# Performance work log

Hardware: AMD Instinct MI355X
Metric: run time of the kernel (lower is better)

## Reference

```python
import jax, jax.numpy as jnp
import numpy as np

N = 100000      # nodes
E = 1600000     # edges (unique, no self-loops)
DIN = 128
DOUT = 128


def _make_edges():
    """Unique undirected edges, no self-loops, ring guarantees min degree 2.
    Ensures dense-adjacency semantics == edge-list segment-sum semantics."""
    rng = np.random.default_rng(0)
    ring = np.stack([np.arange(N, dtype=np.int64), (np.arange(N, dtype=np.int64) + 1) % N], axis=1)
    ring = np.sort(ring, axis=1)  # canonical (min,max)
    ring_keys = ring[:, 0] * N + ring[:, 1]
    cand = rng.integers(0, N, size=(3 * E, 2), dtype=np.int64)
    cand = cand[cand[:, 0] != cand[:, 1]]
    cand = np.sort(cand, axis=1)
    keys = cand[:, 0] * N + cand[:, 1]
    _, idx = np.unique(keys, return_index=True)
    cand = cand[np.sort(idx)]
    cand = cand[~np.isin(cand[:, 0] * N + cand[:, 1], ring_keys)][: E - N]
    edges = np.concatenate([ring, cand], axis=0)  # [E, 2]
    return edges.T  # [2, E]


def setup_inputs() -> dict:
    key = jax.random.key(0)
    kx, kw = jax.random.split(key)
    X = jax.random.normal(kx, (N, DIN), dtype=jnp.float32)
    # kaiming_normal_ default (fan_in mode): std = sqrt(2 / fan_in)
    W = jax.random.normal(kw, (DIN, DOUT), dtype=jnp.float32) * np.float32(np.sqrt(2.0 / DIN))
    edge_list = jnp.asarray(_make_edges(), dtype=jnp.int64)
    return {"X": X, "W": W, "edge_list": edge_list}


def reference(X, W, edge_list):
    src, dst = edge_list[0], edge_list[1]
    n = X.shape[0]
    ones = jnp.ones(src.shape[0], dtype=X.dtype)
    # D: each edge increments both endpoint degrees (matches the torch loop)
    deg = jnp.zeros((n,), X.dtype).at[src].add(ones).at[dst].add(ones)
    # A_hat @ X = symmetric neighbor aggregation + self (identity)
    agg = jnp.zeros_like(X).at[dst].add(X[src]).at[src].add(X[dst]) + X
    # D^-1 is inverse of diagonal -> elementwise reciprocal
    z = (agg / deg[:, None]) @ W
    return jax.nn.relu(z)
```

## Files before the change

### kernel.cpp

```cpp
#include <hip/hip_runtime.h>
#include <hip/hip_fp16.h>


#define DFEAT 128
#define BSH 7
#define BNODES (1 << BSH)
#define NBMAX 800
#define EPB 8192
#define SORT_CAP 6144
#define EPT (SORT_CAP / 1024)

typedef __attribute__((ext_vector_type(8))) short short8;
typedef __attribute__((ext_vector_type(4))) float f32x4;

__device__ __forceinline__ unsigned short f2bf(float x) {
  unsigned u = __float_as_uint(x);
  return (unsigned short)((u + 0x7FFFu + ((u >> 16) & 1u)) >> 16);
}
__device__ __forceinline__ __half2 u2h(unsigned x) {
  union { unsigned u; __half2 h; } c; c.u = x; return c.h;
}

__global__ void init_kernel(const int* el32, int* gcur, int* flag, int NB) {
  int i = blockIdx.x * blockDim.x + threadIdx.x;
  if (i < NB) gcur[i] = 0;
  if (i == 0) flag[0] = (el32[1] == 0 && el32[3] == 0) ? 1 : 0;
}

__device__ __forceinline__ int edge_at(const void* el, long long i, int mode64) {
  if (mode64) return (int)((const long long*)el)[i];
  return ((const int*)el)[i];
}

__global__ __launch_bounds__(1024) void scatter_kernel(const void* el,
                                                       const int* __restrict__ flag,
                                                       int* __restrict__ gcur,
                                                       unsigned int* __restrict__ bucket,
                                                       int E, int NB) {
  __shared__ int lh[NBMAX];
  __shared__ int lb[NBMAX];
  int t = threadIdx.x;
  for (int i = t; i < NB; i += 1024) lh[i] = 0;
  __syncthreads();
  int m = flag[0];
  long long e0 = (long long)blockIdx.x * EPB + t;
  int s[8], d[8];
#pragma unroll
  for (int r = 0; r < 8; r++) {
    long long e = e0 + r * 1024;
    if (e < E) {
      s[r] = edge_at(el, e, m);
      d[r] = edge_at(el, (long long)E + e, m);
    } else {
      s[r] = -1;
    }
  }
#pragma unroll
  for (int r = 0; r < 8; r++) {
    if (s[r] >= 0) {
      atomicAdd(&lh[s[r] >> BSH], 1);
      atomicAdd(&lh[d[r] >> BSH], 1);
    }
  }
  __syncthreads();
  for (int i = t; i < NB; i += 1024) {
    int c = lh[i];
    lb[i] = c ? atomicAdd(&gcur[i], c) : 0;
  }
  __syncthreads();
  for (int i = t; i < NB; i += 1024) lh[i] = 0;
  __syncthreads();
#pragma unroll
  for (int r = 0; r < 8; r++) {
    if (s[r] >= 0) {
      int bs = s[r] >> BSH, bd = d[r] >> BSH;
      int ps = lb[bs] + atomicAdd(&lh[bs], 1);
      if (ps < SORT_CAP)
        bucket[(long long)bs * SORT_CAP + ps] =
            ((unsigned)(s[r] & (BNODES - 1)) << 20) | (unsigned)d[r];
      int pd = lb[bd] + atomicAdd(&lh[bd], 1);
      if (pd < SORT_CAP)
        bucket[(long long)bd * SORT_CAP + pd] =
            ((unsigned)(d[r] & (BNODES - 1)) << 20) | (unsigned)s[r];
    }
  }
}

__global__ __launch_bounds__(256) void wfrag_kernel(const float* __restrict__ W,
                                                    unsigned int* __restrict__ Wfrag) {
  int e = blockIdx.x * 256 + threadIdx.x;
  if (e >= 2048) return;
  int lane = e & 63;
  int nt = (e >> 6) & 7;
  int kc = e >> 9;
  int k0 = kc * 32 + (lane >> 4) * 8;
  int col = nt * 16 + (lane & 15);
  unsigned int o[4];
#pragma unroll
  for (int jj = 0; jj < 4; jj++) {
    unsigned short lo = f2bf(W[(k0 + 2 * jj) * DFEAT + col]);
    unsigned short hi = f2bf(W[(k0 + 2 * jj + 1) * DFEAT + col]);
    o[jj] = (unsigned)lo | ((unsigned)hi << 16);
  }
  uint4* dst = (uint4*)Wfrag;
  uint4 v; v.x = o[0]; v.y = o[1]; v.z = o[2]; v.w = o[3];
  dst[e] = v;
}

__global__ __launch_bounds__(256) void gemm_kernel(const float* __restrict__ X,
                                                   const short8* __restrict__ Wfrag,
                                                   __half* __restrict__ Yh, int n) {
  int wave = threadIdx.x >> 6;
  int lane = threadIdx.x & 63;
  int row0 = (blockIdx.x * 4 + wave) * 16;
  if (row0 >= n) return;

  int rowA = row0 + (lane & 15);
  if (rowA >= n) rowA = n - 1;
  const float4* Xrow = (const float4*)(X + (long long)rowA * DFEAT);
  int koff = (lane >> 4) * 2;

  f32x4 acc[8];
#pragma unroll
  for (int ntp = 0; ntp < 8; ntp++) acc[ntp] = (f32x4){0.f, 0.f, 0.f, 0.f};

#pragma unroll
  for (int kc = 0; kc < 4; kc++) {
    float4 xa = Xrow[kc * 8 + koff];
    float4 xb = Xrow[kc * 8 + koff + 1];
    short8 a8;
    a8[0] = (short)f2bf(xa.x); a8[1] = (short)f2bf(xa.y);
    a8[2] = (short)f2bf(xa.z); a8[3] = (short)f2bf(xa.w);
    a8[4] = (short)f2bf(xb.x); a8[5] = (short)f2bf(xb.y);
    a8[6] = (short)f2bf(xb.z); a8[7] = (short)f2bf(xb.w);
#pragma unroll
    for (int nt = 0; nt < 8; nt++) {
      short8 b8 = Wfrag[(kc * 8 + nt) * 64 + lane];
      acc[nt] = __builtin_amdgcn_mfma_f32_16x16x32_bf16(a8, b8, acc[nt], 0, 0, 0);
    }
  }

  int rbase = row0 + (lane >> 4) * 4;
  int cbase = lane & 15;
#pragma unroll
  for (int nt = 0; nt < 8; nt++) {
#pragma unroll
    for (int r = 0; r < 4; r++) {
      int row = rbase + r;
      if (row < n)
        Yh[(long long)row * DFEAT + nt * 16 + cbase] = __float2half(acc[nt][r]);
    }
  }
}

__global__ __launch_bounds__(1024) void gather_fused(
    const unsigned int* __restrict__ bucket,
    const int* __restrict__ gcur,
    const unsigned int* __restrict__ Yh,
    float2* __restrict__ out2, int n) {
  __shared__ int srt[SORT_CAP];
  __shared__ int h[BNODES], pref[BNODES], cur[BNODES], scn[BNODES];
  int b = blockIdx.x, t = threadIdx.x;
  int cnt = gcur[b]; if (cnt > SORT_CAP) cnt = SORT_CAP;
  long long base = (long long)b * SORT_CAP;

  if (t < BNODES) h[t] = 0;
  __syncthreads();

  unsigned ent[EPT];
#pragma unroll
  for (int r = 0; r < EPT; r++) {
    int i = t + r * 1024;
    if (i < cnt) {
      unsigned e = bucket[base + i];
      ent[r] = e;
      atomicAdd(&h[e >> 20], 1);
    } else {
      ent[r] = 0xFFFFFFFFu;
    }
  }
  __syncthreads();

  int v = (t < BNODES) ? h[t] : 0;
  if (t < BNODES) scn[t] = v;
  __syncthreads();
  for (int dd = 1; dd < BNODES; dd <<= 1) {
    int a = (t < BNODES && t >= dd) ? scn[t - dd] : 0;
    __syncthreads();
    if (t < BNODES) scn[t] += a;
    __syncthreads();
  }
  if (t < BNODES) { pref[t] = scn[t] - v; cur[t] = scn[t] - v; }
  __syncthreads();

#pragma unroll
  for (int r = 0; r < EPT; r++) {
    unsigned e = ent[r];
    if (e != 0xFFFFFFFFu) {
      int p = atomicAdd(&cur[e >> 20], 1);
      srt[p] = (int)(e & 0xFFFFFu);
    }
  }
  __syncthreads();

  int wave = t >> 6, lane = t & 63;
  int node0 = b << BSH;
#pragma unroll 1
  for (int q = 0; q < 8; q++) {
    int r = wave * 8 + q;
    int node = node0 + r;
    if (node >= n) break;
    int st = pref[r], len = h[r];
    __half2 acc0 = u2h(Yh[(long long)node * 64 + lane]);
    __half2 acc1 = u2h(0);

    for (int bb = 0; bb < len; bb += 64) {
      int c2 = len - bb; if (c2 > 64) c2 = 64;
      int idx = (lane < c2) ? srt[st + bb + lane] : 0;
      int tt = 0;
      for (; tt + 8 <= c2; tt += 8) {
        unsigned vv[8];
#pragma unroll
        for (int u = 0; u < 8; u++) {
          int j = __shfl(idx, tt + u);
          vv[u] = Yh[(long long)j * 64 + lane];
        }
        acc0 = __hadd2(acc0, u2h(vv[0])); acc1 = __hadd2(acc1, u2h(vv[1]));
        acc0 = __hadd2(acc0, u2h(vv[2])); acc1 = __hadd2(acc1, u2h(vv[3]));
        acc0 = __hadd2(acc0, u2h(vv[4])); acc1 = __hadd2(acc1, u2h(vv[5]));
        acc0 = __hadd2(acc0, u2h(vv[6])); acc1 = __hadd2(acc1, u2h(vv[7]));
      }
      for (; tt < c2; tt++) {
        int j = __shfl(idx, tt);
        acc0 = __hadd2(acc0, u2h(Yh[(long long)j * 64 + lane]));
      }
    }

    float2 f0 = __half22float2(acc0);
    float2 f1 = __half22float2(acc1);
    float inv = 1.0f / (float)len;
    float2 o;
    o.x = (f0.x + f1.x) * inv;
    o.y = (f0.y + f1.y) * inv;
    o.x = o.x > 0.f ? o.x : 0.f;
    o.y = o.y > 0.f ? o.y : 0.f;
    out2[(long long)node * 64 + lane] = o;
  }
}

extern "C" void kernel_launch(void* const* d_in, const int* in_sizes, int n_in,
                              void* d_out, int out_size, void* d_ws, size_t ws_size,
                              hipStream_t stream) {
  const float* X = (const float*)d_in[0];
  const float* W = (const float*)d_in[1];
  const void* el = d_in[2];
  float* out = (float*)d_out;

  int n = in_sizes[0] / DFEAT;
  int E = in_sizes[2] / 2;
  int NB = (n + BNODES - 1) >> BSH;

  char* p = (char*)d_ws;
  auto alloc = [&](size_t bytes) -> char* {
    char* q = p;
    p += (bytes + 511) & ~(size_t)511;
    return q;
  };
  int* gcur = (int*)alloc((size_t)NBMAX * 4);
  int* flag = (int*)alloc(64);
  unsigned int* bucket = (unsigned int*)alloc((size_t)NBMAX * SORT_CAP * 4);
  unsigned int* Wfrag = (unsigned int*)alloc((size_t)2048 * 16);
  __half* Yh = (__half*)alloc((size_t)n * DFEAT * 2);

  int eblocks = (E + EPB - 1) / EPB;

  init_kernel<<<(NBMAX + 255) / 256, 256, 0, stream>>>((const int*)el, gcur, flag, NB);
  scatter_kernel<<<eblocks, 1024, 0, stream>>>(el, flag, gcur, bucket, E, NB);
  wfrag_kernel<<<8, 256, 0, stream>>>(W, Wfrag);
  gemm_kernel<<<(n + 63) / 64, 256, 0, stream>>>(X, (const short8*)Wfrag, Yh, n);
  gather_fused<<<NB, 1024, 0, stream>>>(bucket, gcur, (const unsigned int*)Yh,
                                        (float2*)out, n);
}
```

Baseline: 275.6 us.

## Window-partition neighbor lists so gather waves sweep source windows for cache locality

A new sort kernel orders each node bucket's neighbors by a (node, source-window) key and writes per-node, per-window offsets and degrees to global memory. The gather kernel then gives each wave 17 nodes and walks the 16 source windows in order, so concurrent gathers touch one window of Yh at a time and stay in L2. The W-fragment kernel is merged into setup, and scatter uses 4 edges per thread instead of 8. The cost is an extra kernel and pass over the buckets. The gather also loses its 8-way unrolled independent loads, which may lower memory-level parallelism.

Result: slower. 551.4 us (+100.0%).

```diff
diff --git a/kernel.cpp b/kernel.cpp
--- a/kernel.cpp
+++ b/kernel.cpp
@@ -6,9 +6,14 @@
 #define BSH 7
 #define BNODES (1 << BSH)
 #define NBMAX 800
-#define EPB 8192
+#define EPT_SC 4
+#define EPB (1024 * EPT_SC)
 #define SORT_CAP 6144
-#define EPT (SORT_CAP / 1024)
+#define WSH 13
+#define NWSLOT 16
+#define KBINS (BNODES * NWSLOT)
+#define NPW 17
+#define GBLK 1536
 
 typedef __attribute__((ext_vector_type(8))) short short8;
 typedef __attribute__((ext_vector_type(4))) float f32x4;
@@ -21,10 +26,30 @@
   union { unsigned u; __half2 h; } c; c.u = x; return c.h;
 }
 
-__global__ void init_kernel(const int* el32, int* gcur, int* flag, int NB) {
-  int i = blockIdx.x * blockDim.x + threadIdx.x;
-  if (i < NB) gcur[i] = 0;
-  if (i == 0) flag[0] = (el32[1] == 0 && el32[3] == 0) ? 1 : 0;
+__global__ __launch_bounds__(256) void setup_kernel(const int* el32, int* gcur,
+                                                    int* flag,
+                                                    const float* __restrict__ W,
+                                                    unsigned int* __restrict__ Wfrag) {
+  int e = blockIdx.x * 256 + threadIdx.x;
+  if (e < NBMAX) gcur[e] = 0;
+  if (e == 0) flag[0] = (el32[1] == 0 && el32[3] == 0) ? 1 : 0;
+  if (e < 2048) {
+    int lane = e & 63;
+    int nt = (e >> 6) & 7;
+    int kc = e >> 9;
+    int k0 = kc * 32 + (lane >> 4) * 8;
+    int col = nt * 16 + (lane & 15);
+    unsigned int o[4];
+#pragma unroll
+    for (int jj = 0; jj < 4; jj++) {
+      unsigned short lo = f2bf(W[(k0 + 2 * jj) * DFEAT + col]);
+      unsigned short hi = f2bf(W[(k0 + 2 * jj + 1) * DFEAT + col]);
+      o[jj] = (unsigned)lo | ((unsigned)hi << 16);
+    }
+    uint4* dst = (uint4*)Wfrag;
+    uint4 v; v.x = o[0]; v.y = o[1]; v.z = o[2]; v.w = o[3];
+    dst[e] = v;
+  }
 }
 
 __device__ __forceinline__ int edge_at(const void* el, long long i, int mode64) {
@@ -44,9 +69,9 @@
   __syncthreads();
   int m = flag[0];
   long long e0 = (long long)blockIdx.x * EPB + t;
-  int s[8], d[8];
-#pragma unroll
-  for (int r = 0; r < 8; r++) {
+  int s[EPT_SC], d[EPT_SC];
+#pragma unroll
+  for (int r = 0; r < EPT_SC; r++) {
     long long e = e0 + r * 1024;
     if (e < E) {
       s[r] = edge_at(el, e, m);
@@ -56,7 +81,7 @@
     }
   }
 #pragma unroll
-  for (int r = 0; r < 8; r++) {
+  for (int r = 0; r < EPT_SC; r++) {
     if (s[r] >= 0) {
       atomicAdd(&lh[s[r] >> BSH], 1);
       atomicAdd(&lh[d[r] >> BSH], 1);
@@ -71,7 +96,7 @@
   for (int i = t; i < NB; i += 1024) lh[i] = 0;
   __syncthreads();
 #pragma unroll
-  for (int r = 0; r < 8; r++) {
+  for (int r = 0; r < EPT_SC; r++) {
     if (s[r] >= 0) {
       int bs = s[r] >> BSH, bd = d[r] >> BSH;
       int ps = lb[bs] + atomicAdd(&lh[bs], 1);
@@ -86,25 +111,64 @@
   }
 }
 
-__global__ __launch_bounds__(256) void wfrag_kernel(const float* __restrict__ W,
-                                                    unsigned int* __restrict__ Wfrag) {
-  int e = blockIdx.x * 256 + threadIdx.x;
-  if (e >= 2048) return;
-  int lane = e & 63;
-  int nt = (e >> 6) & 7;
-  int kc = e >> 9;
-  int k0 = kc * 32 + (lane >> 4) * 8;
-  int col = nt * 16 + (lane & 15);
-  unsigned int o[4];
-#pragma unroll
-  for (int jj = 0; jj < 4; jj++) {
-    unsigned short lo = f2bf(W[(k0 + 2 * jj) * DFEAT + col]);
-    unsigned short hi = f2bf(W[(k0 + 2 * jj + 1) * DFEAT + col]);
-    o[jj] = (unsigned)lo | ((unsigned)hi << 16);
-  }
-  uint4* dst = (uint4*)Wfrag;
-  uint4 v; v.x = o[0]; v.y = o[1]; v.z = o[2]; v.w = o[3];
-  dst[e] = v;
+__global__ __launch_bounds__(1024) void sortwin_kernel(unsigned int* __restrict__ bucket,
+                                                       const int* __restrict__ gcur,
+                                                       int2* __restrict__ pw,
+                                                       int* __restrict__ degg,
+                                                       int n) {
+  __shared__ int srt[SORT_CAP];
+  __shared__ int h2[KBINS], pr2[KBINS], cur2[KBINS];
+  __shared__ int wsc[1024];
+  int b = blockIdx.x, t = threadIdx.x;
+  int cnt = gcur[b]; if (cnt > SORT_CAP) cnt = SORT_CAP;
+  long long base = (long long)b * SORT_CAP;
+
+  h2[t] = 0; h2[t + 1024] = 0;
+  __syncthreads();
+  for (int i = t; i < cnt; i += 1024) {
+    unsigned e = bucket[base + i];
+    int key = (int)((e >> 20) << 4) | (int)((e & 0xFFFFFu) >> WSH);
+    atomicAdd(&h2[key], 1);
+  }
+  __syncthreads();
+  int a0 = h2[2 * t], a1 = h2[2 * t + 1];
+  int s = a0 + a1;
+  wsc[t] = s;
+  __syncthreads();
+  for (int dd = 1; dd < 1024; dd <<= 1) {
+    int aa = (t >= dd) ? wsc[t - dd] : 0;
+    __syncthreads();
+    wsc[t] += aa;
+    __syncthreads();
+  }
+  int excl = wsc[t] - s;
+  pr2[2 * t] = excl;          cur2[2 * t] = excl;
+  pr2[2 * t + 1] = excl + a0; cur2[2 * t + 1] = excl + a0;
+  __syncthreads();
+  for (int i = t; i < cnt; i += 1024) {
+    unsigned e = bucket[base + i];
+    int key = (int)((e >> 20) << 4) | (int)((e & 0xFFFFFu) >> WSH);
+    int p = atomicAdd(&cur2[key], 1);
+    srt[p] = (int)(e & 0xFFFFFu);
+  }
+  __syncthreads();
+  for (int i = t; i < cnt; i += 1024) bucket[base + i] = (unsigned)srt[i];
+  int node0 = b << BSH;
+  for (int i = t; i < KBINS; i += 1024) {
+    int node = node0 + (i >> 4);
+    if (node < n)
+      pw[((long long)node << 4) | (i & 15)] =
+          make_int2((int)(base + pr2[i]), h2[i]);
+  }
+  if (t < BNODES) {
+    int node = node0 + t;
+    if (node < n) {
+      int sdeg = 0;
+#pragma unroll
+      for (int d2 = 0; d2 < NWSLOT; d2++) sdeg += h2[(t << 4) | d2];
+      degg[node] = sdeg;
+    }
+  }
 }
 
 __global__ __launch_bounds__(256) void gemm_kernel(const float* __restrict__ X,
@@ -153,98 +217,55 @@
   }
 }
 
-__global__ __launch_bounds__(1024) void gather_fused(
-    const unsigned int* __restrict__ bucket,
-    const int* __restrict__ gcur,
+__global__ __launch_bounds__(256, 6) void gatherw_kernel(
     const unsigned int* __restrict__ Yh,
+    const int2* __restrict__ pw,
+    const int* __restrict__ degg,
+    const unsigned int* __restrict__ adj,
     float2* __restrict__ out2, int n) {
-  __shared__ int srt[SORT_CAP];
-  __shared__ int h[BNODES], pref[BNODES], cur[BNODES], scn[BNODES];
-  int b = blockIdx.x, t = threadIdx.x;
-  int cnt = gcur[b]; if (cnt > SORT_CAP) cnt = SORT_CAP;
-  long long base = (long long)b * SORT_CAP;
-
-  if (t < BNODES) h[t] = 0;
-  __syncthreads();
-
-  unsigned ent[EPT];
-#pragma unroll
-  for (int r = 0; r < EPT; r++) {
-    int i = t + r * 1024;
-    if (i < cnt) {
-      unsigned e = bucket[base + i];
-      ent[r] = e;
-      atomicAdd(&h[e >> 20], 1);
-    } else {
-      ent[r] = 0xFFFFFFFFu;
-    }
-  }
-  __syncthreads();
-
-  int v = (t < BNODES) ? h[t] : 0;
-  if (t < BNODES) scn[t] = v;
-  __syncthreads();
-  for (int dd = 1; dd < BNODES; dd <<= 1) {
-    int a = (t < BNODES && t >= dd) ? scn[t - dd] : 0;
-    __syncthreads();
-    if (t < BNODES) scn[t] += a;
-    __syncthreads();
-  }
-  if (t < BNODES) { pref[t] = scn[t] - v; cur[t] = scn[t] - v; }
-  __syncthreads();
-
-#pragma unroll
-  for (int r = 0; r < EPT; r++) {
-    unsigned e = ent[r];
-    if (e != 0xFFFFFFFFu) {
-      int p = atomicAdd(&cur[e >> 20], 1);
-      srt[p] = (int)(e & 0xFFFFFu);
-    }
-  }
-  __syncthreads();
-
-  int wave = t >> 6, lane = t & 63;
-  int node0 = b << BSH;
-#pragma unroll 1
-  for (int q = 0; q < 8; q++) {
-    int r = wave * 8 + q;
-    int node = node0 + r;
-    if (node >= n) break;
-    int st = pref[r], len = h[r];
-    __half2 acc0 = u2h(Yh[(long long)node * 64 + lane]);
-    __half2 acc1 = u2h(0);
-
-    for (int bb = 0; bb < len; bb += 64) {
-      int c2 = len - bb; if (c2 > 64) c2 = 64;
-      int idx = (lane < c2) ? srt[st + bb + lane] : 0;
-      int tt = 0;
-      for (; tt + 8 <= c2; tt += 8) {
-        unsigned vv[8];
-#pragma unroll
-        for (int u = 0; u < 8; u++) {
-          int j = __shfl(idx, tt + u);
-          vv[u] = Yh[(long long)j * 64 + lane];
+  int g = (int)((blockIdx.x * (long long)blockDim.x + threadIdx.x) >> 6);
+  int lane = threadIdx.x & 63;
+  int nb0 = g * NPW;
+  if (nb0 >= n) return;
+  int nwin = (n + (1 << WSH) - 1) >> WSH;
+
+  __half2 acc[NPW];
+#pragma unroll
+  for (int k = 0; k < NPW; k++) {
+    int nd = nb0 + k;
+    acc[k] = (nd < n) ? u2h(Yh[(long long)nd * 64 + lane]) : u2h(0u);
+  }
+
+  for (int d = 0; d < nwin; d++) {
+#pragma unroll
+    for (int k = 0; k < NPW; k++) {
+      int nd = nb0 + k;
+      if (nd >= n) continue;
+      int2 sl = pw[((long long)nd << 4) | d];
+      int st = sl.x, ln = sl.y;
+      for (int bb = 0; bb < ln; bb += 64) {
+        int c2 = ln - bb; if (c2 > 64) c2 = 64;
+        int idx = (lane < c2) ? (int)adj[st + bb + lane] : 0;
+        for (int tt = 0; tt < c2; tt++) {
+          int j = __shfl(idx, tt);
+          acc[k] = __hadd2(acc[k], u2h(Yh[(long long)j * 64 + lane]));
         }
-        acc0 = __hadd2(acc0, u2h(vv[0])); acc1 = __hadd2(acc1, u2h(vv[1]));
-        acc0 = __hadd2(acc0, u2h(vv[2])); acc1 = __hadd2(acc1, u2h(vv[3]));
-        acc0 = __hadd2(acc0, u2h(vv[4])); acc1 = __hadd2(acc1, u2h(vv[5]));
-        acc0 = __hadd2(acc0, u2h(vv[6])); acc1 = __hadd2(acc1, u2h(vv[7]));
       }
-      for (; tt < c2; tt++) {
-        int j = __shfl(idx, tt);
-        acc0 = __hadd2(acc0, u2h(Yh[(long long)j * 64 + lane]));
-      }
-    }
-
-    float2 f0 = __half22float2(acc0);
-    float2 f1 = __half22float2(acc1);
-    float inv = 1.0f / (float)len;
+    }
+  }
+
+#pragma unroll
+  for (int k = 0; k < NPW; k++) {
+    int nd = nb0 + k;
+    if (nd >= n) continue;
+    float2 f = __half22float2(acc[k]);
+    float inv = 1.0f / (float)degg[nd];
     float2 o;
-    o.x = (f0.x + f1.x) * inv;
-    o.y = (f0.y + f1.y) * inv;
+    o.x = f.x * inv;
+    o.y = f.y * inv;
     o.x = o.x > 0.f ? o.x : 0.f;
     o.y = o.y > 0.f ? o.y : 0.f;
-    out2[(long long)node * 64 + lane] = o;
+    out2[(long long)nd * 64 + lane] = o;
   }
 }
 
@@ -269,15 +290,17 @@
   int* gcur = (int*)alloc((size_t)NBMAX * 4);
   int* flag = (int*)alloc(64);
   unsigned int* bucket = (unsigned int*)alloc((size_t)NBMAX * SORT_CAP * 4);
+  int2* pw   = (int2*)alloc((size_t)n * NWSLOT * 8);
+  int* degg  = (int*)alloc((size_t)n * 4);
   unsigned int* Wfrag = (unsigned int*)alloc((size_t)2048 * 16);
   __half* Yh = (__half*)alloc((size_t)n * DFEAT * 2);
 
   int eblocks = (E + EPB - 1) / EPB;
 
-  init_kernel<<<(NBMAX + 255) / 256, 256, 0, stream>>>((const int*)el, gcur, flag, NB);
+  setup_kernel<<<8, 256, 0, stream>>>((const int*)el, gcur, flag, W, Wfrag);
   scatter_kernel<<<eblocks, 1024, 0, stream>>>(el, flag, gcur, bucket, E, NB);
-  wfrag_kernel<<<8, 256, 0, stream>>>(W, Wfrag);
+  sortwin_kernel<<<NB, 1024, 0, stream>>>(bucket, gcur, pw, degg, n);
   gemm_kernel<<<(n + 63) / 64, 256, 0, stream>>>(X, (const short8*)Wfrag, Yh, n);
-  gather_fused<<<NB, 1024, 0, stream>>>(bucket, gcur, (const unsigned int*)Yh,
-                                        (float2*)out, n);
-}
+  gatherw_kernel<<<GBLK, 256, 0, stream>>>((const unsigned int*)Yh, pw, degg,
+                                           bucket, (float2*)out, n);
+}
```
